# Kernel optimization log

Hardware: AMD Instinct MI355X
Metric: run time of the kernel (lower is better)

The kernel has to match this reference:

```python
import jax, jax.numpy as jnp
import numpy as np

B, HH, WW = 4, 112, 112
DIM, NH, WS, SHIFT = 384, 12, 7, 3
N = WS * WS
HD = DIM // NH
SCALE = HD ** -0.5
HID = DIM * 4
NW = (HH // WS) * (WW // WS)


def _ln(x, w, b):
    m = x.mean(-1, keepdims=True)
    v = ((x - m) ** 2).mean(-1, keepdims=True)
    return (x - m) / jnp.sqrt(v + 1e-5) * w + b


def _win_part(x):  # (B,H,W,C) -> (B*nW, N, C)
    x = x.reshape(B, HH // WS, WS, WW // WS, WS, DIM).transpose(0, 1, 3, 2, 4, 5)
    return x.reshape(-1, N, DIM)


def _win_rev(w):  # (B*nW, N, C) -> (B,H,W,C)
    x = w.reshape(B, HH // WS, WW // WS, WS, WS, DIM).transpose(0, 1, 3, 2, 4, 5)
    return x.reshape(B, HH, WW, DIM)


def _rel_index():
    c = np.arange(WS)
    coords = np.stack(np.meshgrid(c, c, indexing='ij')).reshape(2, -1)
    rel = (coords[:, :, None] - coords[:, None, :]).transpose(1, 2, 0).copy()
    rel[:, :, 0] += WS - 1
    rel[:, :, 1] += WS - 1
    rel[:, :, 0] *= 2 * WS - 1
    return rel.sum(-1)  # (N, N)


def _attn_mask():
    img = np.zeros((HH, WW))
    cnt = 0
    for hs in (slice(0, -WS), slice(-WS, -SHIFT), slice(-SHIFT, None)):
        for ws_ in (slice(0, -WS), slice(-WS, -SHIFT), slice(-SHIFT, None)):
            img[hs, ws_] = cnt
            cnt += 1
    mw = img.reshape(HH // WS, WS, WW // WS, WS).transpose(0, 2, 1, 3).reshape(-1, N)
    am = mw[:, None, :] - mw[:, :, None]
    return np.where(am != 0, -100.0, 0.0).astype(np.float32)  # (nW, N, N)


def setup_inputs():
    key = jax.random.key(0)
    ks = iter(jax.random.split(key, 32))
    rn = lambda shape, s=0.02: jax.random.normal(next(ks), shape, jnp.float32) * s
    return {
        'branch_1': jax.random.normal(next(ks), (B, HH * WW, DIM), jnp.float32),
        'branch_2': jax.random.normal(next(ks), (B, HH * WW, DIM), jnp.float32),
        'mask_matrix': jnp.asarray(_attn_mask()),
        'rpi': jnp.asarray(_rel_index(), jnp.int32),
        'n1w1': jnp.ones((DIM,)), 'n1b1': jnp.zeros((DIM,)),
        'n1w2': jnp.ones((DIM,)), 'n1b2': jnp.zeros((DIM,)),
        'qw1': rn((3 * DIM, DIM)), 'qb1': jnp.zeros((3 * DIM,)),
        'qw2': rn((3 * DIM, DIM)), 'qb2': jnp.zeros((3 * DIM,)),
        'rpb1': rn(((2 * WS - 1) ** 2, NH)), 'rpb2': rn(((2 * WS - 1) ** 2, NH)),
        'pw1': rn((DIM, DIM)), 'pb1': jnp.zeros((DIM,)),
        'pw2': rn((DIM, DIM)), 'pb2': jnp.zeros((DIM,)),
        'n2w1': jnp.ones((DIM,)), 'n2b1': jnp.zeros((DIM,)),
        'n2w2': jnp.ones((DIM,)), 'n2b2': jnp.zeros((DIM,)),
        'm1fc1w': rn((HID, DIM)), 'm1fc1b': jnp.zeros((HID,)),
        'm1fc2w': rn((DIM, HID)), 'm1fc2b': jnp.zeros((DIM,)),
        'm2fc1w': rn((HID, DIM)), 'm2fc1b': jnp.zeros((HID,)),
        'm2fc2w': rn((DIM, HID)), 'm2fc2b': jnp.zeros((DIM,)),
    }


def _cross_attn(x1, x2, mask, rpi, qw1, qb1, qw2, qb2, rpb1, rpb2, pw1, pb1, pw2, pb2):
    Bw = x1.shape[0]

    def qkv(x, w, b):
        t = (x @ w.T + b).reshape(Bw, N, 3, NH, HD).transpose(2, 0, 3, 1, 4)
        return t[0], t[1], t[2]

    q1, k1, v1 = qkv(x1, qw1, qb1)
    q2, k2, v2 = qkv(x2, qw2, qb2)
    a1 = (q2 * SCALE) @ jnp.swapaxes(k1, -2, -1)  # (Bw, NH, N, N)
    a2 = (q1 * SCALE) @ jnp.swapaxes(k2, -2, -1)
    b1 = rpb1[rpi].transpose(2, 0, 1)  # (NH, N, N)
    b2 = rpb2[rpi].transpose(2, 0, 1)
    a1 = a1 + b1[None]
    a2 = a2 + b2[None]
    nW = mask.shape[0]
    a1 = (a1.reshape(Bw // nW, nW, NH, N, N) + mask[None, :, None]).reshape(Bw, NH, N, N)
    a2 = (a2.reshape(Bw // nW, nW, NH, N, N) + mask[None, :, None]).reshape(Bw, NH, N, N)
    a1 = jax.nn.softmax(a1, axis=-1)
    a2 = jax.nn.softmax(a2, axis=-1)
    o1 = (a1 @ v1).transpose(0, 2, 1, 3).reshape(Bw, N, DIM) @ pw1.T + pb1
    o2 = (a2 @ v2).transpose(0, 2, 1, 3).reshape(Bw, N, DIM) @ pw2.T + pb2
    del o2
    return o1, o1  # faithful to original: it returns [branch_1, branch_1]


def _mlp(x, w1, b1, w2, b2):
    return jax.nn.gelu(x @ w1.T + b1, approximate=False) @ w2.T + b2


def reference(branch_1, branch_2, mask_matrix, rpi, n1w1, n1b1, n1w2, n1b2,
              qw1, qb1, qw2, qb2, rpb1, rpb2, pw1, pb1, pw2, pb2,
              n2w1, n2b1, n2w2, n2b2,
              m1fc1w, m1fc1b, m1fc2w, m1fc2b, m2fc1w, m2fc1b, m2fc2w, m2fc2b):
    s1, s2 = branch_1, branch_2
    x1 = _ln(branch_1, n1w1, n1b1).reshape(B, HH, WW, DIM)
    x2 = _ln(branch_2, n1w2, n1b2).reshape(B, HH, WW, DIM)
    # cyclic shift (shift_size > 0; H,W divisible by window_size so no padding)
    x1 = jnp.roll(x1, (-SHIFT, -SHIFT), (1, 2))
    x2 = jnp.roll(x2, (-SHIFT, -SHIFT), (1, 2))
    w1, w2 = _win_part(x1), _win_part(x2)
    o1, o2 = _cross_attn(w1, w2, mask_matrix, rpi, qw1, qb1, qw2, qb2,
                         rpb1, rpb2, pw1, pb1, pw2, pb2)
    y1 = jnp.roll(_win_rev(o1), (SHIFT, SHIFT), (1, 2)).reshape(B, HH * WW, DIM)
    y2 = jnp.roll(_win_rev(o2), (SHIFT, SHIFT), (1, 2)).reshape(B, HH * WW, DIM)
    b1 = s1 + y1
    b2 = s2 + y2
    out1 = b1 + _mlp(_ln(b1, n2w1, n2b1), m1fc1w, m1fc1b, m1fc2w, m1fc2b)
    out2 = b2 + _mlp(_ln(b2, n2w2, n2b2), m2fc1w, m2fc1b, m2fc2w, m2fc2b)
    return out1, out2
```

## Files before the change

kernel.cpp:

```cpp
#include <hip/hip_runtime.h>
#include <math.h>

#define DEV __device__ __forceinline__

typedef __attribute__((ext_vector_type(8))) unsigned short u16x8;
typedef __attribute__((ext_vector_type(8))) __bf16 bf16x8;
typedef __attribute__((ext_vector_type(4))) float f32x4;

static constexpr int TOK = 50176;
static constexpr int DIMC = 384;
static constexpr float QSCALE = 0.17677669529663687f;

DEV unsigned short f2bf(float f) {
  union { float f; unsigned u; } v; v.f = f;
  unsigned r = v.u + 0x7fffu + ((v.u >> 16) & 1u);
  return (unsigned short)(r >> 16);
}

DEV f32x4 mfma16(bf16x8 a, bf16x8 b, f32x4 c) {
  return __builtin_amdgcn_mfma_f32_16x16x32_bf16(a, b, c, 0, 0, 0);
}

DEV void gload_lds16(const void* g, void* lds) {
  __builtin_amdgcn_global_load_lds(
      (const __attribute__((address_space(1))) void*)g,
      (__attribute__((address_space(3))) void*)lds, 16, 0, 0);
}

__global__ __launch_bounds__(256) void w2bf_kern(const float* __restrict__ in,
                                                 unsigned short* __restrict__ out, int n) {
  int i = blockIdx.x * 256 + threadIdx.x;
  if (i < n) out[i] = f2bf(in[i]);
}

template<bool WINDOW>
__global__ __launch_bounds__(256) void ln_kern(const float* __restrict__ in,
                                               const float* __restrict__ gw,
                                               const float* __restrict__ gb,
                                               unsigned short* __restrict__ out) {
  const int row = blockIdx.x * 4 + (threadIdx.x >> 6);
  const int l = threadIdx.x & 63;
  int src = row;
  if (WINDOW) {
    const int wq = row / 49, nn = row - wq * 49;
    const int bb = wq >> 8, wi = wq & 255;
    int hh = (wi >> 4) * 7 + nn / 7 + 3;        if (hh >= 112) hh -= 112;
    int cc = (wi & 15) * 7 + (nn - (nn / 7) * 7) + 3; if (cc >= 112) cc -= 112;
    src = bb * 12544 + hh * 112 + cc;
  }
  const float* x = in + (size_t)src * DIMC;
  float v[6]; float s = 0.f, s2 = 0.f;
#pragma unroll
  for (int j = 0; j < 6; ++j) { float t = x[l + 64 * j]; v[j] = t; s += t; s2 += t * t; }
#pragma unroll
  for (int d = 1; d < 64; d <<= 1) { s += __shfl_xor(s, d); s2 += __shfl_xor(s2, d); }
  const float mean = s * (1.f / 384.f);
  const float var = s2 * (1.f / 384.f) - mean * mean;
  const float rs = rsqrtf(var + 1e-5f);
#pragma unroll
  for (int j = 0; j < 6; ++j) {
    int c = l + 64 * j;
    out[(size_t)row * DIMC + c] = f2bf((v[j] - mean) * rs * gw[c] + gb[c]);
  }
}

enum { E_BF16 = 0, E_BF16_SCALE = 1, E_SCATTER = 2, E_GELU = 3, E_RESOUT = 4 };

template<int EPI>
__global__ __launch_bounds__(256) void gemm_bt(
    const unsigned short* __restrict__ A, const unsigned short* __restrict__ W,
    const float* __restrict__ bias, int K, int N,
    unsigned short* __restrict__ outb,
    float* __restrict__ outf1, float* __restrict__ outf2,
    const float* __restrict__ res1, const float* __restrict__ res2) {
  __shared__ __align__(16) unsigned short sA[2][128 * 64];
  __shared__ __align__(16) unsigned short sB[2][128 * 64];
  const int t = threadIdx.x;
  const int wv = t >> 6, l = t & 63;
  const int wm = (wv >> 1) * 64, wn = (wv & 1) * 64;
  const int m0 = blockIdx.x * 128, n0 = blockIdx.y * 128;
  const int srow = t >> 3;
  const int scol = ((t & 7) ^ (srow & 7)) * 8;

  f32x4 acc[4][4];
  const f32x4 fzero = {0.f, 0.f, 0.f, 0.f};
#pragma unroll
  for (int i = 0; i < 4; ++i)
#pragma unroll
    for (int j = 0; j < 4; ++j) acc[i][j] = fzero;

  const unsigned short* gA = A + (size_t)(m0 + srow) * K + scol;
  const unsigned short* gB = W + (size_t)(n0 + srow) * K + scol;
  const int ldsW = wv * 512;

  const int g = l >> 4, lr = l & 15;
  const int swz = (lr & 7) << 4;

  const int ntt = K >> 6;
#pragma unroll
  for (int it = 0; it < 4; ++it) {
    gload_lds16(gA + (size_t)(it * 32) * K, &sA[0][it * 2048 + ldsW]);
    gload_lds16(gB + (size_t)(it * 32) * K, &sB[0][it * 2048 + ldsW]);
  }
  for (int tt = 0; tt < ntt; ++tt) {
    const int cur = tt & 1;
    if (tt + 1 < ntt) {
      const int kt = (tt + 1) << 6;
#pragma unroll
      for (int it = 0; it < 4; ++it) {
        gload_lds16(gA + (size_t)(it * 32) * K + kt, &sA[cur ^ 1][it * 2048 + ldsW]);
        gload_lds16(gB + (size_t)(it * 32) * K + kt, &sB[cur ^ 1][it * 2048 + ldsW]);
      }
      asm volatile("s_waitcnt vmcnt(8)" ::: "memory");
    } else {
      asm volatile("s_waitcnt vmcnt(0)" ::: "memory");
    }
    __builtin_amdgcn_s_barrier();
    asm volatile("" ::: "memory");
    const char* bA = (const char*)&sA[cur][0];
    const char* bB = (const char*)&sB[cur][0];
#pragma unroll
    for (int ks = 0; ks < 2; ++ks) {
      bf16x8 af[4], bff[4];
      const int cb = (ks * 64 + g * 16) ^ swz;
#pragma unroll
      for (int mt = 0; mt < 4; ++mt)
        af[mt] = *(const bf16x8*)(bA + (wm + mt * 16 + lr) * 128 + cb);
#pragma unroll
      for (int nt2 = 0; nt2 < 4; ++nt2)
        bff[nt2] = *(const bf16x8*)(bB + (wn + nt2 * 16 + lr) * 128 + cb);
#pragma unroll
      for (int mt = 0; mt < 4; ++mt)
#pragma unroll
        for (int nt2 = 0; nt2 < 4; ++nt2)
          acc[mt][nt2] = mfma16(af[mt], bff[nt2], acc[mt][nt2]);
    }
    asm volatile("" ::: "memory");
    __builtin_amdgcn_s_barrier();
  }

  const int col = lr;
#pragma unroll
  for (int mt = 0; mt < 4; ++mt) {
#pragma unroll
    for (int r = 0; r < 4; ++r) {
      const int m = m0 + wm + mt * 16 + g * 4 + r;
      size_t obase = 0;
      if constexpr (EPI == E_SCATTER) {
        int wq = m / 49, nn = m - wq * 49;
        int bb = wq >> 8, wi = wq & 255;
        int hh = (wi >> 4) * 7 + nn / 7 + 3;        if (hh >= 112) hh -= 112;
        int cc = (wi & 15) * 7 + (nn - (nn / 7) * 7) + 3; if (cc >= 112) cc -= 112;
        obase = ((size_t)bb * 12544 + hh * 112 + cc) * 384;
      }
#pragma unroll
      for (int nt2 = 0; nt2 < 4; ++nt2) {
        const int j = n0 + wn + nt2 * 16 + col;
        float v = acc[mt][nt2][r] + bias[j];
        if constexpr (EPI == E_BF16) {
          outb[(size_t)m * N + j] = f2bf(v);
        } else if constexpr (EPI == E_BF16_SCALE) {
          outb[(size_t)m * N + j] = f2bf(v * QSCALE);
        } else if constexpr (EPI == E_GELU) {
          outb[(size_t)m * N + j] = f2bf(0.5f * v * (1.f + erff(v * 0.70710678118654752f)));
        } else if constexpr (EPI == E_SCATTER) {
          outf1[obase + j] = res1[obase + j] + v;
          outf2[obase + j] = res2[obase + j] + v;
        } else {
          outf1[(size_t)m * N + j] = v + res1[(size_t)m * N + j];
        }
      }
    }
  }
}

__global__ __launch_bounds__(256) void attn_kern(
    const unsigned short* __restrict__ q2,
    const unsigned short* __restrict__ kv1,
    const int* __restrict__ rpi,
    const float* __restrict__ mask,
    const float* __restrict__ rpb,
    unsigned short* __restrict__ o) {
  const int w = blockIdx.x, h = blockIdx.y;
  __shared__ __align__(16) unsigned short sQ[64 * 32];
  __shared__ __align__(16) unsigned short sK[64 * 32];
  __shared__ __align__(16) unsigned short sVT[32 * 64];
  __shared__ __align__(16) unsigned short sP[64 * 64];
  const int t = threadIdx.x, wv = t >> 6, l = t & 63;
  const int r = t >> 2, c = (t & 3) * 8;
  const u16x8 z8 = {0, 0, 0, 0, 0, 0, 0, 0};
  if (r < 49) {
    *(u16x8*)&sQ[r * 32 + c] = *(const u16x8*)&q2[((size_t)w * 49 + r) * 384 + h * 32 + c];
    *(u16x8*)&sK[r * 32 + c] = *(const u16x8*)&kv1[((size_t)w * 49 + r) * 768 + h * 32 + c];
    u16x8 vv = *(const u16x8*)&kv1[((size_t)w * 49 + r) * 768 + 384 + h * 32 + c];
#pragma unroll
    for (int e = 0; e < 8; ++e) sVT[(c + e) * 64 + r] = vv[e];
  } else {
    *(u16x8*)&sQ[r * 32 + c] = z8;
    *(u16x8*)&sK[r * 32 + c] = z8;
#pragma unroll
    for (int e = 0; e < 8; ++e) sVT[(c + e) * 64 + r] = 0;
  }
  __syncthreads();

  const int g = l >> 4, col = l & 15;
  const f32x4 fzero = {0.f, 0.f, 0.f, 0.f};
  bf16x8 aq = *(const bf16x8*)&sQ[(wv * 16 + col) * 32 + g * 8];
  f32x4 s[4];
#pragma unroll
  for (int nt = 0; nt < 4; ++nt) {
    bf16x8 bk = *(const bf16x8*)&sK[(nt * 16 + col) * 32 + g * 8];
    s[nt] = mfma16(aq, bk, fzero);
  }

  const int wi = w & 255;
  float p[4][4];
#pragma unroll
  for (int rr = 0; rr < 4; ++rr) {
    const int i = wv * 16 + g * 4 + rr;
    float mx = -1e30f;
#pragma unroll
    for (int nt = 0; nt < 4; ++nt) {
      const int j = nt * 16 + col;
      float val = -1e9f;
      if (i < 49 && j < 49)
        val = s[nt][rr] + rpb[rpi[i * 49 + j] * 12 + h] + mask[((size_t)wi * 49 + i) * 49 + j];
      p[nt][rr] = val;
      mx = fmaxf(mx, val);
    }
#pragma unroll
    for (int d = 1; d < 16; d <<= 1) mx = fmaxf(mx, __shfl_xor(mx, d));
    float sm = 0.f;
#pragma unroll
    for (int nt = 0; nt < 4; ++nt) {
      const int j = nt * 16 + col;
      float e = (j < 49) ? __expf(p[nt][rr] - mx) : 0.f;
      p[nt][rr] = e; sm += e;
    }
#pragma unroll
    for (int d = 1; d < 16; d <<= 1) sm += __shfl_xor(sm, d);
    const float inv = 1.f / sm;
#pragma unroll
    for (int nt = 0; nt < 4; ++nt) p[nt][rr] *= inv;
  }
#pragma unroll
  for (int rr = 0; rr < 4; ++rr) {
    const int i = wv * 16 + g * 4 + rr;
#pragma unroll
    for (int nt = 0; nt < 4; ++nt) sP[i * 64 + nt * 16 + col] = f2bf(p[nt][rr]);
  }
  __syncthreads();

  f32x4 oa[2] = {fzero, fzero};
#pragma unroll
  for (int ks = 0; ks < 2; ++ks) {
    bf16x8 ap = *(const bf16x8*)&sP[(wv * 16 + col) * 64 + ks * 32 + g * 8];
#pragma unroll
    for (int n2 = 0; n2 < 2; ++n2) {
      bf16x8 bv = *(const bf16x8*)&sVT[(n2 * 16 + col) * 64 + ks * 32 + g * 8];
      oa[n2] = mfma16(ap, bv, oa[n2]);
    }
  }
#pragma unroll
  for (int rr = 0; rr < 4; ++rr) {
    const int i = wv * 16 + g * 4 + rr;
    if (i < 49) {
#pragma unroll
      for (int n2 = 0; n2 < 2; ++n2)
        o[((size_t)w * 49 + i) * 384 + h * 32 + n2 * 16 + col] = f2bf(oa[n2][rr]);
    }
  }
}

extern "C" void kernel_launch(void* const* d_in, const int* in_sizes, int n_in,
                              void* d_out, int out_size, void* d_ws, size_t ws_size,
                              hipStream_t stream) {
  (void)in_sizes; (void)n_in; (void)out_size; (void)ws_size;
  const float* s1   = (const float*)d_in[0];
  const float* s2   = (const float*)d_in[1];
  const float* mask = (const float*)d_in[2];
  const int*   rpi  = (const int*)d_in[3];
  const float* n1w1 = (const float*)d_in[4],  *n1b1 = (const float*)d_in[5];
  const float* n1w2 = (const float*)d_in[6],  *n1b2 = (const float*)d_in[7];
  const float* qw1  = (const float*)d_in[8],  *qb1  = (const float*)d_in[9];
  const float* qw2  = (const float*)d_in[10], *qb2  = (const float*)d_in[11];
  const float* rpb1 = (const float*)d_in[12];
  const float* pw1  = (const float*)d_in[14], *pb1  = (const float*)d_in[15];
  const float* n2w1 = (const float*)d_in[18], *n2b1 = (const float*)d_in[19];
  const float* n2w2 = (const float*)d_in[20], *n2b2 = (const float*)d_in[21];
  const float* m1fc1w = (const float*)d_in[22], *m1fc1b = (const float*)d_in[23];
  const float* m1fc2w = (const float*)d_in[24], *m1fc2b = (const float*)d_in[25];
  const float* m2fc1w = (const float*)d_in[26], *m2fc1b = (const float*)d_in[27];
  const float* m2fc2w = (const float*)d_in[28], *m2fc2b = (const float*)d_in[29];

  char* ws = (char*)d_ws;
  const size_t S1 = (size_t)TOK * DIMC * 2;
  unsigned short* x1w  = (unsigned short*)(ws);
  unsigned short* x2w  = (unsigned short*)(ws + S1);
  unsigned short* kv1  = (unsigned short*)(ws + 2 * S1);
  unsigned short* q2b  = (unsigned short*)(ws + 4 * S1);
  unsigned short* obuf = x1w;
  unsigned short* hbuf = x2w;
  unsigned short* xm   = x1w;
  char* wp = ws + 5 * S1;
  unsigned short* wq1b = (unsigned short*)(wp);
  unsigned short* wq2b = (unsigned short*)(wp + 589824);
  unsigned short* wp1b = (unsigned short*)(wp + 884736);
  unsigned short* wf11 = (unsigned short*)(wp + 1179648);
  unsigned short* wf12 = (unsigned short*)(wp + 2359296);
  unsigned short* wf21 = (unsigned short*)(wp + 3538944);
  unsigned short* wf22 = (unsigned short*)(wp + 4718592);

  float* outf = (float*)d_out;
  float* b1 = outf;
  float* b2 = outf + (size_t)19267584;

  w2bf_kern<<<(294912 + 255) / 256, 256, 0, stream>>>(qw1 + 384 * 384, wq1b, 294912);
  w2bf_kern<<<(147456 + 255) / 256, 256, 0, stream>>>(qw2, wq2b, 147456);
  w2bf_kern<<<(147456 + 255) / 256, 256, 0, stream>>>(pw1, wp1b, 147456);
  w2bf_kern<<<(589824 + 255) / 256, 256, 0, stream>>>(m1fc1w, wf11, 589824);
  w2bf_kern<<<(589824 + 255) / 256, 256, 0, stream>>>(m1fc2w, wf12, 589824);
  w2bf_kern<<<(589824 + 255) / 256, 256, 0, stream>>>(m2fc1w, wf21, 589824);
  w2bf_kern<<<(589824 + 255) / 256, 256, 0, stream>>>(m2fc2w, wf22, 589824);

  ln_kern<true><<<TOK / 4, 256, 0, stream>>>(s1, n1w1, n1b1, x1w);
  ln_kern<true><<<TOK / 4, 256, 0, stream>>>(s2, n1w2, n1b2, x2w);

  gemm_bt<E_BF16><<<dim3(392, 6), 256, 0, stream>>>(x1w, wq1b, qb1 + 384, 384, 768,
                                                    kv1, nullptr, nullptr, nullptr, nullptr);
  gemm_bt<E_BF16_SCALE><<<dim3(392, 3), 256, 0, stream>>>(x2w, wq2b, qb2, 384, 384,
                                                          q2b, nullptr, nullptr, nullptr, nullptr);
  attn_kern<<<dim3(1024, 12), 256, 0, stream>>>(q2b, kv1, rpi, mask, rpb1, obuf);

  gemm_bt<E_SCATTER><<<dim3(392, 3), 256, 0, stream>>>(obuf, wp1b, pb1, 384, 384,
                                                       nullptr, b1, b2, s1, s2);
  ln_kern<false><<<TOK / 4, 256, 0, stream>>>(b1, n2w1, n2b1, xm);
  gemm_bt<E_GELU><<<dim3(392, 12), 256, 0, stream>>>(xm, wf11, m1fc1b, 384, 1536,
                                                     hbuf, nullptr, nullptr, nullptr, nullptr);
  gemm_bt<E_RESOUT><<<dim3(392, 3), 256, 0, stream>>>(hbuf, wf12, m1fc2b, 1536, 384,
                                                      nullptr, b1, nullptr, b1, nullptr);
  ln_kern<false><<<TOK / 4, 256, 0, stream>>>(b2, n2w2, n2b2, xm);
  gemm_bt<E_GELU><<<dim3(392, 12), 256, 0, stream>>>(xm, wf21, m2fc1b, 384, 1536,
                                                     hbuf, nullptr, nullptr, nullptr, nullptr);
  gemm_bt<E_RESOUT><<<dim3(392, 3), 256, 0, stream>>>(hbuf, wf22, m2fc2b, 1536, 384,
                                                      nullptr, b2, nullptr, b2, nullptr);
}
```

Baseline: 877.3 us.

## Triple-buffer GEMM K-loop, remap blocks per XCD, use tanh-form GELU

```diff
diff --git a/kernel.cpp b/kernel.cpp
--- a/kernel.cpp
+++ b/kernel.cpp
@@ -69,18 +69,24 @@
 template<int EPI>
 __global__ __launch_bounds__(256) void gemm_bt(
     const unsigned short* __restrict__ A, const unsigned short* __restrict__ W,
-    const float* __restrict__ bias, int K, int N,
+    const float* __restrict__ bias, int K, int N, int nbx,
     unsigned short* __restrict__ outb,
     float* __restrict__ outf1, float* __restrict__ outf2,
     const float* __restrict__ res1, const float* __restrict__ res2) {
-  __shared__ __align__(16) unsigned short sA[2][128 * 64];
-  __shared__ __align__(16) unsigned short sB[2][128 * 64];
+  __shared__ __align__(16) unsigned short sA[3][128 * 32];
+  __shared__ __align__(16) unsigned short sB[3][128 * 32];
   const int t = threadIdx.x;
   const int wv = t >> 6, l = t & 63;
   const int wm = (wv >> 1) * 64, wn = (wv & 1) * 64;
-  const int m0 = blockIdx.x * 128, n0 = blockIdx.y * 128;
-  const int srow = t >> 3;
-  const int scol = ((t & 7) ^ (srow & 7)) * 8;
+
+  const int total = gridDim.x;
+  const int q = total >> 3, rr8 = total & 7;
+  const int xcd = blockIdx.x & 7, lid = blockIdx.x >> 3;
+  const int wgid = (xcd < rr8 ? xcd * (q + 1) : rr8 * (q + 1) + (xcd - rr8) * q) + lid;
+  const int n0 = (wgid % nbx) * 128, m0 = (wgid / nbx) * 128;
+
+  const int srow = t >> 2;
+  const int scol = ((t & 3) ^ ((t >> 3) & 3)) * 8;
 
   f32x4 acc[4][4];
   const f32x4 fzero = {0.f, 0.f, 0.f, 0.f};
@@ -94,49 +100,52 @@
   const int ldsW = wv * 512;
 
   const int g = l >> 4, lr = l & 15;
-  const int swz = (lr & 7) << 4;
-
-  const int ntt = K >> 6;
-#pragma unroll
-  for (int it = 0; it < 4; ++it) {
-    gload_lds16(gA + (size_t)(it * 32) * K, &sA[0][it * 2048 + ldsW]);
-    gload_lds16(gB + (size_t)(it * 32) * K, &sB[0][it * 2048 + ldsW]);
+  const int swz = ((lr >> 1) & 3) << 4;
+
+  const int ntt = K >> 5;
+#pragma unroll
+  for (int p = 0; p < 2; ++p) {
+#pragma unroll
+    for (int it = 0; it < 2; ++it) {
+      gload_lds16(gA + (size_t)(it * 64) * K + p * 32, &sA[p][it * 2048 + ldsW]);
+      gload_lds16(gB + (size_t)(it * 64) * K + p * 32, &sB[p][it * 2048 + ldsW]);
+    }
   }
   for (int tt = 0; tt < ntt; ++tt) {
-    const int cur = tt & 1;
     if (tt + 1 < ntt) {
-      const int kt = (tt + 1) << 6;
-#pragma unroll
-      for (int it = 0; it < 4; ++it) {
-        gload_lds16(gA + (size_t)(it * 32) * K + kt, &sA[cur ^ 1][it * 2048 + ldsW]);
-        gload_lds16(gB + (size_t)(it * 32) * K + kt, &sB[cur ^ 1][it * 2048 + ldsW]);
-      }
-      asm volatile("s_waitcnt vmcnt(8)" ::: "memory");
+      asm volatile("s_waitcnt vmcnt(4)" ::: "memory");
     } else {
       asm volatile("s_waitcnt vmcnt(0)" ::: "memory");
     }
     __builtin_amdgcn_s_barrier();
     asm volatile("" ::: "memory");
-    const char* bA = (const char*)&sA[cur][0];
-    const char* bB = (const char*)&sB[cur][0];
-#pragma unroll
-    for (int ks = 0; ks < 2; ++ks) {
-      bf16x8 af[4], bff[4];
-      const int cb = (ks * 64 + g * 16) ^ swz;
-#pragma unroll
-      for (int mt = 0; mt < 4; ++mt)
-        af[mt] = *(const bf16x8*)(bA + (wm + mt * 16 + lr) * 128 + cb);
+    if (tt + 2 < ntt) {
+      const int kt = (tt + 2) << 5;
+      const int b2 = (tt + 2) % 3;
+#pragma unroll
+      for (int it = 0; it < 2; ++it) {
+        gload_lds16(gA + (size_t)(it * 64) * K + kt, &sA[b2][it * 2048 + ldsW]);
+        gload_lds16(gB + (size_t)(it * 64) * K + kt, &sB[b2][it * 2048 + ldsW]);
+      }
+    }
+    const int cb = tt % 3;
+    const char* bA = (const char*)&sA[cb][0];
+    const char* bB = (const char*)&sB[cb][0];
+    bf16x8 af[4], bff[4];
+#pragma unroll
+    for (int mt = 0; mt < 4; ++mt)
+      af[mt] = *(const bf16x8*)(bA + (wm + mt * 16 + lr) * 64 + ((g * 16) ^ swz));
+#pragma unroll
+    for (int nt2 = 0; nt2 < 4; ++nt2)
+      bff[nt2] = *(const bf16x8*)(bB + (wn + nt2 * 16 + lr) * 64 + ((g * 16) ^ swz));
+    __builtin_amdgcn_s_setprio(1);
+#pragma unroll
+    for (int mt = 0; mt < 4; ++mt)
 #pragma unroll
       for (int nt2 = 0; nt2 < 4; ++nt2)
-        bff[nt2] = *(const bf16x8*)(bB + (wn + nt2 * 16 + lr) * 128 + cb);
-#pragma unroll
-      for (int mt = 0; mt < 4; ++mt)
-#pragma unroll
-        for (int nt2 = 0; nt2 < 4; ++nt2)
-          acc[mt][nt2] = mfma16(af[mt], bff[nt2], acc[mt][nt2]);
-    }
+        acc[mt][nt2] = mfma16(af[mt], bff[nt2], acc[mt][nt2]);
+    __builtin_amdgcn_s_setprio(0);
     asm volatile("" ::: "memory");
-    __builtin_amdgcn_s_barrier();
   }
 
   const int col = lr;
@@ -162,7 +171,9 @@
         } else if constexpr (EPI == E_BF16_SCALE) {
           outb[(size_t)m * N + j] = f2bf(v * QSCALE);
         } else if constexpr (EPI == E_GELU) {
-          outb[(size_t)m * N + j] = f2bf(0.5f * v * (1.f + erff(v * 0.70710678118654752f)));
+          float z = v * (1.5957691216057308f + 0.0713548162726009f * v * v);
+          float gg = v / (1.f + __expf(-z));
+          outb[(size_t)m * N + j] = f2bf(gg);
         } else if constexpr (EPI == E_SCATTER) {
           outf1[obase + j] = res1[obase + j] + v;
           outf2[obase + j] = res2[obase + j] + v;
@@ -326,22 +337,22 @@
   ln_kern<true><<<TOK / 4, 256, 0, stream>>>(s1, n1w1, n1b1, x1w);
   ln_kern<true><<<TOK / 4, 256, 0, stream>>>(s2, n1w2, n1b2, x2w);
 
-  gemm_bt<E_BF16><<<dim3(392, 6), 256, 0, stream>>>(x1w, wq1b, qb1 + 384, 384, 768,
-                                                    kv1, nullptr, nullptr, nullptr, nullptr);
-  gemm_bt<E_BF16_SCALE><<<dim3(392, 3), 256, 0, stream>>>(x2w, wq2b, qb2, 384, 384,
-                                                          q2b, nullptr, nullptr, nullptr, nullptr);
+  gemm_bt<E_BF16><<<6 * 392, 256, 0, stream>>>(x1w, wq1b, qb1 + 384, 384, 768, 6,
+                                               kv1, nullptr, nullptr, nullptr, nullptr);
+  gemm_bt<E_BF16_SCALE><<<3 * 392, 256, 0, stream>>>(x2w, wq2b, qb2, 384, 384, 3,
+                                                     q2b, nullptr, nullptr, nullptr, nullptr);
   attn_kern<<<dim3(1024, 12), 256, 0, stream>>>(q2b, kv1, rpi, mask, rpb1, obuf);
 
-  gemm_bt<E_SCATTER><<<dim3(392, 3), 256, 0, stream>>>(obuf, wp1b, pb1, 384, 384,
-                                                       nullptr, b1, b2, s1, s2);
+  gemm_bt<E_SCATTER><<<3 * 392, 256, 0, stream>>>(obuf, wp1b, pb1, 384, 384, 3,
+                                                  nullptr, b1, b2, s1, s2);
   ln_kern<false><<<TOK / 4, 256, 0, stream>>>(b1, n2w1, n2b1, xm);
-  gemm_bt<E_GELU><<<dim3(392, 12), 256, 0, stream>>>(xm, wf11, m1fc1b, 384, 1536,
-                                                     hbuf, nullptr, nullptr, nullptr, nullptr);
-  gemm_bt<E_RESOUT><<<dim3(392, 3), 256, 0, stream>>>(hbuf, wf12, m1fc2b, 1536, 384,
-                                                      nullptr, b1, nullptr, b1, nullptr);
+  gemm_bt<E_GELU><<<12 * 392, 256, 0, stream>>>(xm, wf11, m1fc1b, 384, 1536, 12,
+                                                hbuf, nullptr, nullptr, nullptr, nullptr);
+  gemm_bt<E_RESOUT><<<3 * 392, 256, 0, stream>>>(hbuf, wf12, m1fc2b, 1536, 384, 3,
+                                                 nullptr, b1, nullptr, b1, nullptr);
   ln_kern<false><<<TOK / 4, 256, 0, stream>>>(b2, n2w2, n2b2, xm);
-  gemm_bt<E_GELU><<<dim3(392, 12), 256, 0, stream>>>(xm, wf21, m2fc1b, 384, 1536,
-                                                     hbuf, nullptr, nullptr, nullptr, nullptr);
-  gemm_bt<E_RESOUT><<<dim3(392, 3), 256, 0, stream>>>(hbuf, wf22, m2fc2b, 1536, 384,
-                                                      nullptr, b2, nullptr, b2, nullptr);
-}
+  gemm_bt<E_GELU><<<12 * 392, 256, 0, stream>>>(xm, wf21, m2fc1b, 384, 1536, 12,
+                                                hbuf, nullptr, nullptr, nullptr, nullptr);
+  gemm_bt<E_RESOUT><<<3 * 392, 256, 0, stream>>>(hbuf, wf22, m2fc2b, 1536, 384, 3,
+                                                 nullptr, b2, nullptr, b2, nullptr);
+}
```

Measured after the change: 855.7 us. -2.5%, faster.
